# Performance work log

Measured on AMD Instinct MI355X. Metric: run time of the kernel, lower is better.

Reference implementation:

```python
import jax, jax.numpy as jnp
import numpy as np

N_NODES = 100000


def setup_inputs() -> dict:
    key = jax.random.key(0)
    k1, k2, k3, k4, k5 = jax.random.split(key, 5)
    dim_in, dim_out = 128, 128
    x = jax.random.normal(k1, (N_NODES, dim_in), dtype=jnp.float32)
    edge_index = jax.random.randint(k2, (2, 1600000), 0, N_NODES, dtype=jnp.int64)
    # PyG SAGEConv params: lin_l (neighbor path, with bias), lin_r (root path, no bias)
    s = 1.0 / np.sqrt(dim_in)
    W_l = jax.random.uniform(k3, (dim_in, dim_out), jnp.float32, -s, s)
    b_l = jax.random.uniform(k4, (dim_out,), jnp.float32, -s, s)
    W_r = jax.random.uniform(k5, (dim_in, dim_out), jnp.float32, -s, s)
    return {"x": x, "edge_index": edge_index, "W_l": W_l, "b_l": b_l, "W_r": W_r}


def reference(x, edge_index, W_l, b_l, W_r):
    src, dst = edge_index[0], edge_index[1]
    # mean aggregation of source features onto target nodes
    gathered = x[src]                                   # [E, d_in]
    summed = jax.ops.segment_sum(gathered, dst, num_segments=N_NODES)
    ones = jnp.ones((edge_index.shape[1],), dtype=x.dtype)
    count = jax.ops.segment_sum(ones, dst, num_segments=N_NODES)
    agg = summed / jnp.maximum(count, 1.0)[:, None]     # [N, d_in]
    # out = lin_l(agg) + lin_r(x)
    return agg @ W_l + b_l + x @ W_r
```

## Files before the change

### kernel.cpp

```cpp
#include <hip/hip_runtime.h>

#define N_NODES 100000
#define DIM 128
#define NE 1600000
#define NTILES (N_NODES / 8)
#define GEMM_BLOCKS 2048
#define CHUNK 512
#define NCHUNK ((N_NODES + CHUNK - 1) / CHUNK)

#define WT_BLOCKS 128
#define NCOARSE 391
#define CPAD 16
#define CCAP 4608
#define CB_BLOCKS 512
#define EPA (NE / CB_BLOCKS)
#define BCAP 640
#define NFINE 3125
#define BK_CAP 1024

typedef unsigned short u16;
typedef __attribute__((ext_vector_type(8))) short bf16x8;
typedef __attribute__((ext_vector_type(4))) float f32x4;

__device__ __forceinline__ float bf2f(u16 h) {
  return __uint_as_float(((unsigned int)h) << 16);
}
__device__ __forceinline__ u16 f2bf(float f) {
  unsigned int u = __float_as_uint(f);
  unsigned int lsb = (u >> 16) & 1u;
  u += 0x7fffu + lsb;
  return (u16)(u >> 16);
}


__global__ __launch_bounds__(256) void prep_k(const float* __restrict__ x,
                                              const float* __restrict__ Wl,
                                              const float* __restrict__ Wr,
                                              u16* __restrict__ Ax,
                                              u16* __restrict__ Wt) {
  const int blk = blockIdx.x;
  if (blk < WT_BLOCKS) {
    int idx = blk * 256 + threadIdx.x;
    int n = idx >> 8;
    int k = idx & 255;
    float v = (k < 128) ? Wr[(size_t)k * DIM + n] : Wl[(size_t)(k - 128) * DIM + n];
    Wt[(size_t)n * 256 + k] = f2bf(v);
    return;
  }
  int t = (blk - WT_BLOCKS) * 256 + threadIdx.x;
  int row = t >> 5;
  int c = (t & 31) * 4;
  float4 v = *(const float4*)(x + (size_t)row * DIM + c);
  ushort4 o;
  o.x = f2bf(v.x); o.y = f2bf(v.y); o.z = f2bf(v.z); o.w = f2bf(v.w);
  *(ushort4*)(Ax + (size_t)row * DIM + c) = o;
}

__global__ __launch_bounds__(512) void coarse_bin_k(const int* __restrict__ ei,
                                                    int* __restrict__ curC,
                                                    int* __restrict__ binnedC) {
  __shared__ u16 keyS[EPA];
  __shared__ int recS[EPA];
  __shared__ u16 key2[EPA];
  __shared__ int rec2[EPA];
  __shared__ int hist[NCOARSE];
  __shared__ int off[NCOARSE];
  __shared__ int lcur[NCOARSE];
  __shared__ int gbase[NCOARSE];
  __shared__ int scanb[512];
  const int tid = threadIdx.x;
  const int e0 = blockIdx.x * EPA;

  for (int i = tid; i < NCOARSE; i += 512) hist[i] = 0;
  __syncthreads();
  for (int i = tid; i < EPA; i += 512) {
    int src = ei[e0 + i];
    int dst = ei[NE + e0 + i];
    keyS[i] = (u16)(dst >> 8);
    recS[i] = ((dst & 255) << 17) | src;
    atomicAdd(&hist[dst >> 8], 1);
  }
  __syncthreads();
  int v = (tid < NCOARSE) ? hist[tid] : 0;
  scanb[tid] = v;
  __syncthreads();
  for (int o = 1; o < 512; o <<= 1) {
    int add = (tid >= o) ? scanb[tid - o] : 0;
    __syncthreads();
    scanb[tid] += add;
    __syncthreads();
  }
  if (tid < NCOARSE) {
    int ex = scanb[tid] - v;
    off[tid] = ex;
    lcur[tid] = ex;
    gbase[tid] = v ? atomicAdd(&curC[tid * CPAD], v) : 0;
  }
  __syncthreads();
  for (int i = tid; i < EPA; i += 512) {
    int k = keyS[i];
    int p = atomicAdd(&lcur[k], 1);
    rec2[p] = recS[i];
    key2[p] = (u16)k;
  }
  __syncthreads();
  for (int i = tid; i < EPA; i += 512) {
    int k = key2[i];
    int gp = gbase[k] + (i - off[k]);
    if (gp < CCAP) binnedC[(size_t)k * CCAP + gp] = rec2[i];
  }
}

__global__ __launch_bounds__(256) void fine_bin_k(const int* __restrict__ curC,
                                                  const int* __restrict__ binnedC,
                                                  int* __restrict__ binned,
                                                  int* __restrict__ bcnt) {
  __shared__ int recS[CCAP];
  __shared__ int rec2[CCAP];
  __shared__ int hist[8];
  __shared__ int off[8];
  __shared__ int lcur[8];
  const int c = blockIdx.x;
  const int tid = threadIdx.x;
  int cnt = curC[c * CPAD];
  if (cnt > CCAP) cnt = CCAP;

  if (tid < 8) hist[tid] = 0;
  __syncthreads();
  for (int i = tid; i < cnt; i += 256) {
    int r = binnedC[(size_t)c * CCAP + i];
    recS[i] = r;
    atomicAdd(&hist[r >> 22], 1);
  }
  __syncthreads();
  if (tid < 8) {
    int vv = hist[tid];
    bcnt[c * 8 + tid] = vv > BCAP ? BCAP : vv;
  }
  if (tid == 0) {
    int a = 0;
#pragma unroll
    for (int k = 0; k < 8; ++k) { off[k] = a; lcur[k] = a; a += hist[k]; }
  }
  __syncthreads();
  for (int i = tid; i < cnt; i += 256) {
    int r = recS[i];
    int p = atomicAdd(&lcur[r >> 22], 1);
    rec2[p] = r;
  }
  __syncthreads();
  for (int i = tid; i < cnt; i += 256) {
    int r = rec2[i];
    int k = r >> 22;
    int sl = i - off[k];
    if (sl < BCAP)
      binned[(size_t)(c * 8 + k) * BCAP + sl] = r & 0x3FFFFF;
  }
}

__global__ __launch_bounds__(256) void aggB_k(const int* __restrict__ bcnt,
                                              const int* __restrict__ binned,
                                              const u16* __restrict__ Ax,
                                              u16* __restrict__ Ag) {
  __shared__ int recS[BK_CAP];
  __shared__ int srcS[BK_CAP];
  __shared__ int hist[32];
  __shared__ int off[32];
  __shared__ int curS[32];
  const int b = blockIdx.x;
  const size_t lo = (size_t)b * BCAP;
  int cnt = bcnt[b];
  if (cnt > BK_CAP) cnt = BK_CAP;

  if (threadIdx.x < 32) hist[threadIdx.x] = 0;
  __syncthreads();
  for (int i = threadIdx.x; i < cnt; i += 256) {
    int rec = __builtin_nontemporal_load(&binned[lo + i]);
    recS[i] = rec;
    atomicAdd(&hist[rec >> 17], 1);
  }
  __syncthreads();
  if (threadIdx.x < 32) off[threadIdx.x] = hist[threadIdx.x];
  __syncthreads();
  for (int st = 1; st < 32; st <<= 1) {
    int add = 0;
    if (threadIdx.x < 32 && threadIdx.x >= st) add = off[threadIdx.x - st];
    __syncthreads();
    if (threadIdx.x < 32) off[threadIdx.x] += add;
    __syncthreads();
  }
  if (threadIdx.x < 32) curS[threadIdx.x] = off[threadIdx.x] - hist[threadIdx.x];
  __syncthreads();
  for (int i = threadIdx.x; i < cnt; i += 256) {
    int rec = recS[i];
    int l = atomicAdd(&curS[rec >> 17], 1);
    srcS[l] = (rec & 0x1FFFF) << 7;
  }
  __syncthreads();

  const int wid = threadIdx.x >> 6;
  const int lane = threadIdx.x & 63;
  const int node0 = b * 32;
  for (int ln = wid; ln < 32; ln += 4) {
    int node = node0 + ln;
    int d = hist[ln];
    int e1 = off[ln];
    int j = e1 - d;
    float ax = 0.f, ay = 0.f;
    for (; j + 4 <= e1; j += 4) {
      int s0 = srcS[j], s1 = srcS[j + 1], s2 = srcS[j + 2], s3 = srcS[j + 3];
      unsigned u0 = *(const unsigned*)(Ax + (size_t)(s0 + lane * 2));
      unsigned u1 = *(const unsigned*)(Ax + (size_t)(s1 + lane * 2));
      unsigned u2 = *(const unsigned*)(Ax + (size_t)(s2 + lane * 2));
      unsigned u3 = *(const unsigned*)(Ax + (size_t)(s3 + lane * 2));
      ax += bf2f((u16)u0) + bf2f((u16)u1) + bf2f((u16)u2) + bf2f((u16)u3);
      ay += bf2f((u16)(u0 >> 16)) + bf2f((u16)(u1 >> 16)) +
            bf2f((u16)(u2 >> 16)) + bf2f((u16)(u3 >> 16));
    }
    for (; j < e1; ++j) {
      unsigned u0 = *(const unsigned*)(Ax + (size_t)(srcS[j] + lane * 2));
      ax += bf2f((u16)u0);
      ay += bf2f((u16)(u0 >> 16));
    }
    float scale = 1.0f / fmaxf((float)d, 1.0f);
    unsigned p = (unsigned)f2bf(ax * scale) | ((unsigned)f2bf(ay * scale) << 16);
    *(unsigned*)(Ag + (size_t)node * DIM + lane * 2) = p;
  }
}

__global__ __launch_bounds__(256) void gemm_mfma(const u16* __restrict__ Ax,
                                                 const u16* __restrict__ Ag,
                                                 const u16* __restrict__ Wt,
                                                 const float* __restrict__ bias,
                                                 float* __restrict__ out) {
  const int wave = threadIdx.x >> 6;
  const int lane = threadIdx.x & 63;
  const int m = lane & 15;
  const int q = lane >> 4;
  const int n0 = wave * 32;

  bf16x8 Bf[2][8];
#pragma unroll
  for (int t = 0; t < 2; ++t) {
    const u16* bp = Wt + (size_t)(n0 + t * 16 + m) * 256 + q * 8;
#pragma unroll
    for (int s = 0; s < 8; ++s) Bf[t][s] = *(const bf16x8*)(bp + s * 32);
  }
  const float b0 = bias[n0 + m];
  const float b1 = bias[n0 + 16 + m];

  const int NT = N_NODES / 16;
  int rt = blockIdx.x;
  bf16x8 Ac[8];
  {
    const u16* apx = Ax + (size_t)(rt * 16 + m) * DIM + q * 8;
    const u16* apg = Ag + (size_t)(rt * 16 + m) * DIM + q * 8;
#pragma unroll
    for (int s = 0; s < 4; ++s) Ac[s] = *(const bf16x8*)(apx + s * 32);
#pragma unroll
    for (int s = 4; s < 8; ++s) Ac[s] = *(const bf16x8*)(apg + (s - 4) * 32);
  }
  while (true) {
    int rn = rt + gridDim.x;
    bf16x8 An[8];
    if (rn < NT) {
      const u16* apx = Ax + (size_t)(rn * 16 + m) * DIM + q * 8;
      const u16* apg = Ag + (size_t)(rn * 16 + m) * DIM + q * 8;
#pragma unroll
      for (int s = 0; s < 4; ++s) An[s] = *(const bf16x8*)(apx + s * 32);
#pragma unroll
      for (int s = 4; s < 8; ++s) An[s] = *(const bf16x8*)(apg + (s - 4) * 32);
    }
    f32x4 acc0 = {0.f, 0.f, 0.f, 0.f};
    f32x4 acc1 = {0.f, 0.f, 0.f, 0.f};
#pragma unroll
    for (int s = 0; s < 8; ++s) {
      acc0 = __builtin_amdgcn_mfma_f32_16x16x32_bf16(Ac[s], Bf[0][s], acc0, 0, 0, 0);
      acc1 = __builtin_amdgcn_mfma_f32_16x16x32_bf16(Ac[s], Bf[1][s], acc1, 0, 0, 0);
    }
    float* o = out + (size_t)(rt * 16 + q * 4) * DIM + n0 + m;
#pragma unroll
    for (int r = 0; r < 4; ++r) {
      o[(size_t)r * DIM] = acc0[r] + b0;
      o[(size_t)r * DIM + 16] = acc1[r] + b1;
    }
    if (rn >= NT) break;
#pragma unroll
    for (int s = 0; s < 8; ++s) Ac[s] = An[s];
    rt = rn;
  }
}

__global__ __launch_bounds__(256) void hist_k(const int* __restrict__ ei,
                                              int* __restrict__ deg) {
  int e = blockIdx.x * 256 + threadIdx.x;
  if (e < NE) atomicAdd(&deg[ei[NE + e]], 1);
}

__global__ __launch_bounds__(512) void scan_sum_k(const int* __restrict__ deg,
                                                  int* __restrict__ partials) {
  __shared__ int s[CHUNK];
  int i = blockIdx.x * CHUNK + threadIdx.x;
  s[threadIdx.x] = (i < N_NODES) ? deg[i] : 0;
  __syncthreads();
  for (int off = 256; off > 0; off >>= 1) {
    if (threadIdx.x < off) s[threadIdx.x] += s[threadIdx.x + off];
    __syncthreads();
  }
  if (threadIdx.x == 0) partials[blockIdx.x] = s[0];
}

__global__ __launch_bounds__(256) void scan_part_k(int* __restrict__ partials) {
  __shared__ int s[256];
  int t = threadIdx.x;
  int v = (t < NCHUNK) ? partials[t] : 0;
  s[t] = v;
  __syncthreads();
  for (int off = 1; off < 256; off <<= 1) {
    int add = (t >= off) ? s[t - off] : 0;
    __syncthreads();
    s[t] += add;
    __syncthreads();
  }
  if (t < NCHUNK) partials[t] = s[t] - v;
}

__global__ __launch_bounds__(512) void scan_out_k(const int* __restrict__ deg,
                                                  const int* __restrict__ partials,
                                                  int* __restrict__ offsets,
                                                  int* __restrict__ cursor) {
  __shared__ int s[CHUNK];
  int t = threadIdx.x;
  int i = blockIdx.x * CHUNK + t;
  int v = (i < N_NODES) ? deg[i] : 0;
  s[t] = v;
  __syncthreads();
  for (int off = 1; off < CHUNK; off <<= 1) {
    int add = (t >= off) ? s[t - off] : 0;
    __syncthreads();
    s[t] += add;
    __syncthreads();
  }
  if (i < N_NODES) {
    int excl = partials[blockIdx.x] + s[t] - v;
    offsets[i] = excl;
    cursor[i] = excl;
  }
  if (i == 0) offsets[N_NODES] = NE;
}

__global__ __launch_bounds__(256) void fill_k(const int* __restrict__ ei,
                                              int* __restrict__ cursor,
                                              int* __restrict__ csr) {
  int e = blockIdx.x * 256 + threadIdx.x;
  if (e < NE) {
    int dst = ei[NE + e];
    int pos = atomicAdd(&cursor[dst], 1);
    csr[pos] = ei[e];
  }
}

__global__ __launch_bounds__(256) void agg_f32_k(const int* __restrict__ offsets,
                                                 const int* __restrict__ csr,
                                                 const float* __restrict__ x,
                                                 float* __restrict__ agg) {
  int node = blockIdx.x * 4 + (threadIdx.x >> 6);
  int lane = threadIdx.x & 63;
  int beg = offsets[node], end = offsets[node + 1];
  float ax = 0.f, ay = 0.f;
  int i = beg;
  for (; i + 4 <= end; i += 4) {
    int s0 = csr[i], s1 = csr[i + 1], s2 = csr[i + 2], s3 = csr[i + 3];
    float2 v0 = *(const float2*)(x + (size_t)s0 * DIM + lane * 2);
    float2 v1 = *(const float2*)(x + (size_t)s1 * DIM + lane * 2);
    float2 v2 = *(const float2*)(x + (size_t)s2 * DIM + lane * 2);
    float2 v3 = *(const float2*)(x + (size_t)s3 * DIM + lane * 2);
    ax += v0.x + v1.x + v2.x + v3.x;
    ay += v0.y + v1.y + v2.y + v3.y;
  }
  for (; i < end; ++i) {
    float2 v0 = *(const float2*)(x + (size_t)csr[i] * DIM + lane * 2);
    ax += v0.x;
    ay += v0.y;
  }
  float scale = 1.0f / fmaxf((float)(end - beg), 1.0f);
  float2 r;
  r.x = ax * scale;
  r.y = ay * scale;
  *(float2*)(agg + (size_t)node * DIM + lane * 2) = r;
}

__global__ __launch_bounds__(256) void gemm_xw(const float* __restrict__ x,
                                               const float* __restrict__ W,
                                               const float* __restrict__ b,
                                               float* __restrict__ out) {
  __shared__ float Ws[DIM * DIM];
  for (int i = threadIdx.x; i < DIM * DIM; i += 256) Ws[i] = W[i];
  __syncthreads();
  const int c = threadIdx.x & 127;
  const int half = threadIdx.x >> 7;
  const float bias = b[c];
  for (int tile = blockIdx.x; tile < NTILES; tile += gridDim.x) {
    const int row0 = tile * 8 + half * 4;
    const float* r = x + (size_t)row0 * DIM;
    float a0 = 0.f, a1 = 0.f, a2 = 0.f, a3 = 0.f;
#pragma unroll 8
    for (int k4 = 0; k4 < 32; ++k4) {
      float4 p0 = *(const float4*)(r + 0 * DIM + k4 * 4);
      float4 p1 = *(const float4*)(r + 1 * DIM + k4 * 4);
      float4 p2 = *(const float4*)(r + 2 * DIM + k4 * 4);
      float4 p3 = *(const float4*)(r + 3 * DIM + k4 * 4);
      const float* wp = &Ws[k4 * 4 * DIM + c];
      float w0 = wp[0 * DIM], w1 = wp[1 * DIM], w2 = wp[2 * DIM], w3 = wp[3 * DIM];
      a0 += p0.x * w0 + p0.y * w1 + p0.z * w2 + p0.w * w3;
      a1 += p1.x * w0 + p1.y * w1 + p1.z * w2 + p1.w * w3;
      a2 += p2.x * w0 + p2.y * w1 + p2.z * w2 + p2.w * w3;
      a3 += p3.x * w0 + p3.y * w1 + p3.z * w2 + p3.w * w3;
    }
    out[(size_t)(row0 + 0) * DIM + c] = a0 + bias;
    out[(size_t)(row0 + 1) * DIM + c] = a1 + bias;
    out[(size_t)(row0 + 2) * DIM + c] = a2 + bias;
    out[(size_t)(row0 + 3) * DIM + c] = a3 + bias;
  }
}

__global__ __launch_bounds__(256) void gemm_aw(const float* __restrict__ agg,
                                               const float* __restrict__ W,
                                               float* __restrict__ out) {
  __shared__ float Ws[DIM * DIM];
  for (int i = threadIdx.x; i < DIM * DIM; i += 256) Ws[i] = W[i];
  __syncthreads();
  const int c = threadIdx.x & 127;
  const int half = threadIdx.x >> 7;
  for (int tile = blockIdx.x; tile < NTILES; tile += gridDim.x) {
    const int row0 = tile * 8 + half * 4;
    const float* r = agg + (size_t)row0 * DIM;
    float a0 = 0.f, a1 = 0.f, a2 = 0.f, a3 = 0.f;
#pragma unroll 8
    for (int k4 = 0; k4 < 32; ++k4) {
      float4 p0 = *(const float4*)(r + 0 * DIM + k4 * 4);
      float4 p1 = *(const float4*)(r + 1 * DIM + k4 * 4);
      float4 p2 = *(const float4*)(r + 2 * DIM + k4 * 4);
      float4 p3 = *(const float4*)(r + 3 * DIM + k4 * 4);
      const float* wp = &Ws[k4 * 4 * DIM + c];
      float w0 = wp[0 * DIM], w1 = wp[1 * DIM], w2 = wp[2 * DIM], w3 = wp[3 * DIM];
      a0 += p0.x * w0 + p0.y * w1 + p0.z * w2 + p0.w * w3;
      a1 += p1.x * w0 + p1.y * w1 + p1.z * w2 + p1.w * w3;
      a2 += p2.x * w0 + p2.y * w1 + p2.z * w2 + p2.w * w3;
      a3 += p3.x * w0 + p3.y * w1 + p3.z * w2 + p3.w * w3;
    }
    out[(size_t)(row0 + 0) * DIM + c] += a0;
    out[(size_t)(row0 + 1) * DIM + c] += a1;
    out[(size_t)(row0 + 2) * DIM + c] += a2;
    out[(size_t)(row0 + 3) * DIM + c] += a3;
  }
}

extern "C" void kernel_launch(void* const* d_in, const int* in_sizes, int n_in,
                              void* d_out, int out_size, void* d_ws, size_t ws_size,
                              hipStream_t stream) {
  const float* x  = (const float*)d_in[0];
  const int*   ei = (const int*)d_in[1];
  const float* Wl = (const float*)d_in[2];
  const float* bl = (const float*)d_in[3];
  const float* Wr = (const float*)d_in[4];
  float* out = (float*)d_out;

  u16* Ax       = (u16*)d_ws;
  u16* Ag       = Ax + (size_t)N_NODES * DIM;
  u16* Wt       = Ag + (size_t)N_NODES * DIM;
  int* curC     = (int*)(Wt + 128 * 256);
  int* bcnt     = curC + NCOARSE * CPAD;
  int* binnedC  = (int*)d_out;
  int* binned   = binnedC + (size_t)NCOARSE * CCAP;
  size_t needed = (size_t)N_NODES * DIM * 2 * 2 + 65536 +
                  (NCOARSE * CPAD + 3200) * 4;

  if (ws_size >= needed) {
    hipMemsetAsync(curC, 0, NCOARSE * CPAD * sizeof(int), stream);
    hipLaunchKernelGGL(prep_k, dim3(WT_BLOCKS + 12500), dim3(256), 0, stream,
                       x, Wl, Wr, Ax, Wt);
    hipLaunchKernelGGL(coarse_bin_k, dim3(CB_BLOCKS), dim3(512), 0, stream,
                       ei, curC, binnedC);
    hipLaunchKernelGGL(fine_bin_k, dim3(NCOARSE), dim3(256), 0, stream,
                       curC, binnedC, binned, bcnt);
    hipLaunchKernelGGL(aggB_k, dim3(NFINE), dim3(256), 0, stream,
                       bcnt, binned, Ax, Ag);
    hipLaunchKernelGGL(gemm_mfma, dim3(1250), dim3(256), 0, stream,
                       Ax, Ag, Wt, bl, out);
  } else {
    int* deg2      = (int*)d_ws;
    int* offsets2  = deg2 + N_NODES;
    int* partials2 = offsets2 + 100004;
    int* csr2      = partials2 + 256;
    float* agg     = (float*)(csr2 + NE);
    hipMemsetAsync(deg2, 0, (size_t)N_NODES * sizeof(int), stream);
    hipLaunchKernelGGL(hist_k, dim3((NE + 255) / 256), dim3(256), 0, stream, ei, deg2);
    hipLaunchKernelGGL(scan_sum_k, dim3(NCHUNK), dim3(CHUNK), 0, stream, deg2, partials2);
    hipLaunchKernelGGL(scan_part_k, dim3(1), dim3(256), 0, stream, partials2);
    hipLaunchKernelGGL(scan_out_k, dim3(NCHUNK), dim3(CHUNK), 0, stream,
                       deg2, partials2, offsets2, deg2);
    hipLaunchKernelGGL(fill_k, dim3((NE + 255) / 256), dim3(256), 0, stream,
                       ei, deg2, csr2);
    hipLaunchKernelGGL(agg_f32_k, dim3(N_NODES / 4), dim3(256), 0, stream,
                       offsets2, csr2, x, agg);
    hipLaunchKernelGGL(gemm_xw, dim3(GEMM_BLOCKS), dim3(256), 0, stream,
                       x, Wr, bl, out);
    hipLaunchKernelGGL(gemm_aw, dim3(GEMM_BLOCKS), dim3(256), 0, stream,
                       agg, Wl, out);
  }
}
```

Baseline: 236.7 us.

## Fuse weight/feature bf16 conversion into coarse binning kernel and add nontemporal accesses

Merges the prep kernel (weight transpose and x-to-bf16 conversion) into the coarse binning kernel as extra blocks, saving a launch and letting the two independent stages overlap. Adds nontemporal loads and stores on streaming edge, feature and output accesses to reduce cache pollution. Splits the aggregation kernel into two launches over halves of the bins. The fused kernel's large static shared memory now applies to the simple conversion blocks, which may limit their occupancy.

```diff
diff --git a/kernel.cpp b/kernel.cpp
--- a/kernel.cpp
+++ b/kernel.cpp
@@ -8,15 +8,17 @@
 #define CHUNK 512
 #define NCHUNK ((N_NODES + CHUNK - 1) / CHUNK)
 
-#define WT_BLOCKS 128
 #define NCOARSE 391
 #define CPAD 16
 #define CCAP 4608
 #define CB_BLOCKS 512
 #define EPA (NE / CB_BLOCKS)
+#define WT_BLOCKS2 64
+#define CONV_BLOCKS 6250
 #define BCAP 640
 #define NFINE 3125
 #define BK_CAP 1024
+#define AGG_SPLIT 1563
 
 typedef unsigned short u16;
 typedef __attribute__((ext_vector_type(8))) short bf16x8;
@@ -33,32 +35,14 @@
 }
 
 
-__global__ __launch_bounds__(256) void prep_k(const float* __restrict__ x,
-                                              const float* __restrict__ Wl,
-                                              const float* __restrict__ Wr,
-                                              u16* __restrict__ Ax,
-                                              u16* __restrict__ Wt) {
-  const int blk = blockIdx.x;
-  if (blk < WT_BLOCKS) {
-    int idx = blk * 256 + threadIdx.x;
-    int n = idx >> 8;
-    int k = idx & 255;
-    float v = (k < 128) ? Wr[(size_t)k * DIM + n] : Wl[(size_t)(k - 128) * DIM + n];
-    Wt[(size_t)n * 256 + k] = f2bf(v);
-    return;
-  }
-  int t = (blk - WT_BLOCKS) * 256 + threadIdx.x;
-  int row = t >> 5;
-  int c = (t & 31) * 4;
-  float4 v = *(const float4*)(x + (size_t)row * DIM + c);
-  ushort4 o;
-  o.x = f2bf(v.x); o.y = f2bf(v.y); o.z = f2bf(v.z); o.w = f2bf(v.w);
-  *(ushort4*)(Ax + (size_t)row * DIM + c) = o;
-}
-
-__global__ __launch_bounds__(512) void coarse_bin_k(const int* __restrict__ ei,
-                                                    int* __restrict__ curC,
-                                                    int* __restrict__ binnedC) {
+__global__ __launch_bounds__(512) void binprep_k(const int* __restrict__ ei,
+                                                 const float* __restrict__ x,
+                                                 const float* __restrict__ Wl,
+                                                 const float* __restrict__ Wr,
+                                                 u16* __restrict__ Ax,
+                                                 u16* __restrict__ Wt,
+                                                 int* __restrict__ curC,
+                                                 int* __restrict__ binnedC) {
   __shared__ u16 keyS[EPA];
   __shared__ int recS[EPA];
   __shared__ u16 key2[EPA];
@@ -68,14 +52,34 @@
   __shared__ int lcur[NCOARSE];
   __shared__ int gbase[NCOARSE];
   __shared__ int scanb[512];
+  const int blk = blockIdx.x;
   const int tid = threadIdx.x;
-  const int e0 = blockIdx.x * EPA;
-
+
+  if (blk >= CB_BLOCKS + WT_BLOCKS2) {
+    int t = (blk - CB_BLOCKS - WT_BLOCKS2) * 512 + tid;
+    int row = t >> 5;
+    int c = (t & 31) * 4;
+    f32x4 v = __builtin_nontemporal_load((const f32x4*)(x + (size_t)row * DIM + c));
+    ushort4 o;
+    o.x = f2bf(v[0]); o.y = f2bf(v[1]); o.z = f2bf(v[2]); o.w = f2bf(v[3]);
+    *(ushort4*)(Ax + (size_t)row * DIM + c) = o;
+    return;
+  }
+  if (blk >= CB_BLOCKS) {
+    int idx = (blk - CB_BLOCKS) * 512 + tid;
+    int n = idx >> 8;
+    int k = idx & 255;
+    float v = (k < 128) ? Wr[(size_t)k * DIM + n] : Wl[(size_t)(k - 128) * DIM + n];
+    Wt[(size_t)n * 256 + k] = f2bf(v);
+    return;
+  }
+
+  const int e0 = blk * EPA;
   for (int i = tid; i < NCOARSE; i += 512) hist[i] = 0;
   __syncthreads();
   for (int i = tid; i < EPA; i += 512) {
-    int src = ei[e0 + i];
-    int dst = ei[NE + e0 + i];
+    int src = __builtin_nontemporal_load(&ei[e0 + i]);
+    int dst = __builtin_nontemporal_load(&ei[NE + e0 + i]);
     keyS[i] = (u16)(dst >> 8);
     recS[i] = ((dst & 255) << 17) | src;
     atomicAdd(&hist[dst >> 8], 1);
@@ -128,7 +132,7 @@
   if (tid < 8) hist[tid] = 0;
   __syncthreads();
   for (int i = tid; i < cnt; i += 256) {
-    int r = binnedC[(size_t)c * CCAP + i];
+    int r = __builtin_nontemporal_load(&binnedC[(size_t)c * CCAP + i]);
     recS[i] = r;
     atomicAdd(&hist[r >> 22], 1);
   }
@@ -158,7 +162,8 @@
   }
 }
 
-__global__ __launch_bounds__(256) void aggB_k(const int* __restrict__ bcnt,
+__global__ __launch_bounds__(256) void aggB_k(int base,
+                                              const int* __restrict__ bcnt,
                                               const int* __restrict__ binned,
                                               const u16* __restrict__ Ax,
                                               u16* __restrict__ Ag) {
@@ -167,7 +172,7 @@
   __shared__ int hist[32];
   __shared__ int off[32];
   __shared__ int curS[32];
-  const int b = blockIdx.x;
+  const int b = base + blockIdx.x;
   const size_t lo = (size_t)b * BCAP;
   int cnt = bcnt[b];
   if (cnt > BK_CAP) cnt = BK_CAP;
@@ -256,9 +261,9 @@
     const u16* apx = Ax + (size_t)(rt * 16 + m) * DIM + q * 8;
     const u16* apg = Ag + (size_t)(rt * 16 + m) * DIM + q * 8;
 #pragma unroll
-    for (int s = 0; s < 4; ++s) Ac[s] = *(const bf16x8*)(apx + s * 32);
-#pragma unroll
-    for (int s = 4; s < 8; ++s) Ac[s] = *(const bf16x8*)(apg + (s - 4) * 32);
+    for (int s = 0; s < 4; ++s) Ac[s] = __builtin_nontemporal_load((const bf16x8*)(apx + s * 32));
+#pragma unroll
+    for (int s = 4; s < 8; ++s) Ac[s] = __builtin_nontemporal_load((const bf16x8*)(apg + (s - 4) * 32));
   }
   while (true) {
     int rn = rt + gridDim.x;
@@ -267,9 +272,9 @@
       const u16* apx = Ax + (size_t)(rn * 16 + m) * DIM + q * 8;
       const u16* apg = Ag + (size_t)(rn * 16 + m) * DIM + q * 8;
 #pragma unroll
-      for (int s = 0; s < 4; ++s) An[s] = *(const bf16x8*)(apx + s * 32);
-#pragma unroll
-      for (int s = 4; s < 8; ++s) An[s] = *(const bf16x8*)(apg + (s - 4) * 32);
+      for (int s = 0; s < 4; ++s) An[s] = __builtin_nontemporal_load((const bf16x8*)(apx + s * 32));
+#pragma unroll
+      for (int s = 4; s < 8; ++s) An[s] = __builtin_nontemporal_load((const bf16x8*)(apg + (s - 4) * 32));
     }
     f32x4 acc0 = {0.f, 0.f, 0.f, 0.f};
     f32x4 acc1 = {0.f, 0.f, 0.f, 0.f};
@@ -281,8 +286,8 @@
     float* o = out + (size_t)(rt * 16 + q * 4) * DIM + n0 + m;
 #pragma unroll
     for (int r = 0; r < 4; ++r) {
-      o[(size_t)r * DIM] = acc0[r] + b0;
-      o[(size_t)r * DIM + 16] = acc1[r] + b1;
+      __builtin_nontemporal_store(acc0[r] + b0, &o[(size_t)r * DIM]);
+      __builtin_nontemporal_store(acc1[r] + b1, &o[(size_t)r * DIM + 16]);
     }
     if (rn >= NT) break;
 #pragma unroll
@@ -478,14 +483,14 @@
 
   if (ws_size >= needed) {
     hipMemsetAsync(curC, 0, NCOARSE * CPAD * sizeof(int), stream);
-    hipLaunchKernelGGL(prep_k, dim3(WT_BLOCKS + 12500), dim3(256), 0, stream,
-                       x, Wl, Wr, Ax, Wt);
-    hipLaunchKernelGGL(coarse_bin_k, dim3(CB_BLOCKS), dim3(512), 0, stream,
-                       ei, curC, binnedC);
+    hipLaunchKernelGGL(binprep_k, dim3(CB_BLOCKS + WT_BLOCKS2 + CONV_BLOCKS),
+                       dim3(512), 0, stream, ei, x, Wl, Wr, Ax, Wt, curC, binnedC);
     hipLaunchKernelGGL(fine_bin_k, dim3(NCOARSE), dim3(256), 0, stream,
                        curC, binnedC, binned, bcnt);
-    hipLaunchKernelGGL(aggB_k, dim3(NFINE), dim3(256), 0, stream,
-                       bcnt, binned, Ax, Ag);
+    hipLaunchKernelGGL(aggB_k, dim3(AGG_SPLIT), dim3(256), 0, stream,
+                       0, bcnt, binned, Ax, Ag);
+    hipLaunchKernelGGL(aggB_k, dim3(NFINE - AGG_SPLIT), dim3(256), 0, stream,
+                       AGG_SPLIT, bcnt, binned, Ax, Ag);
     hipLaunchKernelGGL(gemm_mfma, dim3(1250), dim3(256), 0, stream,
                        Ax, Ag, Wt, bl, out);
   } else {
```

Result: slower. 254.6 us (+7.6%).
